# Optimization experiments

Measured on AMD Instinct MI355X. Metric: run time of the kernel, lower is better.

The kernel has to match this reference:

```python
import jax, jax.numpy as jnp
import numpy as np

B, H, SQ, SK, D = 2, 16, 2048, 2048, 128
SCALE = 0.20884964425119185
P_DROP = 0.125

def setup_inputs() -> dict:
    key = jax.random.key(0)
    k1, k2, k3 = jax.random.split(key, 3)
    x1 = jax.random.normal(k1, (B, H, SQ, D), dtype=jnp.float32)
    x2 = jax.random.normal(k2, (B, H, SK, D), dtype=jnp.float32)
    # inverted dropout mask: 0 with prob p, else 1/(1-p)
    keep = jax.random.uniform(k3, (B, H, SQ, SK)) >= P_DROP
    dropout_mask = keep.astype(jnp.float32) / (1.0 - P_DROP)
    return {"x1": x1, "x2": x2, "dropout_mask": dropout_mask}

def reference(x1, x2, dropout_mask):
    # scores: [B,H,Sq,Sk]
    scores = jnp.einsum('bhqd,bhkd->bhqk', x1, x2) * SCALE
    attn = jax.nn.softmax(scores, axis=-1)
    attn = attn * dropout_mask
    # output: [B,H,Sq,D]
    return jnp.einsum('bhqk,bhkd->bhqd', attn, x2)
```

## Files before the change

kernel.cpp:

```cpp
#include <hip/hip_runtime.h>
#include <hip/hip_bf16.h>

#define SQ 2048
#define SK 2048
#define DD 128
#define NBH 32
#define QBLK 64
#define KBLK 32
#define NKT (SK / KBLK)
#define SCALE 0.20884964425119185f
#define SCL2 (SCALE * 1.4426950408889634f)

typedef __attribute__((ext_vector_type(8))) short short8;
typedef __attribute__((ext_vector_type(4))) float f32x4;
typedef __attribute__((ext_vector_type(4))) unsigned int u32x4;

#define KIMG 8192
#define SMEM_BF 32768
#define KPITCH 272
#define VPITCH 80
#define VOFF_F 8704
#define SMEM_F32 18944

#define GLDS(G, L) __builtin_amdgcn_global_load_lds( \
    (const __attribute__((address_space(1))) unsigned int*)(G), \
    (__attribute__((address_space(3))) unsigned int*)(L), 16, 0, 0)

static __device__ __forceinline__ unsigned int pk_bf16(float lo, float hi) {
    float2 f2; f2.x = lo; f2.y = hi;
    __hip_bfloat162 h = __float22bfloat162_rn(f2);
    union { __hip_bfloat162 h2; unsigned int u; } cv; cv.h2 = h;
    return cv.u;
}

#define SOFTMAX_NAT(PA, SA_, SB_, MCa, MCb, LPART)                             \
  { float p_[8];                                                               \
    p_[0] = __builtin_amdgcn_exp2f(SA_[0]*SCL2);                               \
    p_[1] = __builtin_amdgcn_exp2f(SA_[1]*SCL2);                               \
    p_[2] = __builtin_amdgcn_exp2f(SA_[2]*SCL2);                               \
    p_[3] = __builtin_amdgcn_exp2f(SA_[3]*SCL2);                               \
    p_[4] = __builtin_amdgcn_exp2f(SB_[0]*SCL2);                               \
    p_[5] = __builtin_amdgcn_exp2f(SB_[1]*SCL2);                               \
    p_[6] = __builtin_amdgcn_exp2f(SB_[2]*SCL2);                               \
    p_[7] = __builtin_amdgcn_exp2f(SB_[3]*SCL2);                               \
    LPART += ((p_[0]+p_[1]) + (p_[2]+p_[3])) + ((p_[4]+p_[5]) + (p_[6]+p_[7]));\
    p_[0]*=MCa.x; p_[1]*=MCa.y; p_[2]*=MCa.z; p_[3]*=MCa.w;                    \
    p_[4]*=MCb.x; p_[5]*=MCb.y; p_[6]*=MCb.z; p_[7]*=MCb.w;                    \
    union { unsigned int u[4]; short8 v; } pb_;                                \
    pb_.u[0] = pk_bf16(p_[0],p_[1]); pb_.u[1] = pk_bf16(p_[2],p_[3]);          \
    pb_.u[2] = pk_bf16(p_[4],p_[5]); pb_.u[3] = pk_bf16(p_[6],p_[7]);          \
    PA = pb_.v; }

#define SOFTMAX_PACK(PA, SA_, SB_, MCa, MCb, LPART)                            \
  { float p_[8];                                                               \
    p_[0] = __builtin_amdgcn_exp2f(SA_[0]*SCL2);                               \
    p_[1] = __builtin_amdgcn_exp2f(SA_[1]*SCL2);                               \
    p_[2] = __builtin_amdgcn_exp2f(SA_[2]*SCL2);                               \
    p_[3] = __builtin_amdgcn_exp2f(SA_[3]*SCL2);                               \
    p_[4] = __builtin_amdgcn_exp2f(SB_[0]*SCL2);                               \
    p_[5] = __builtin_amdgcn_exp2f(SB_[1]*SCL2);                               \
    p_[6] = __builtin_amdgcn_exp2f(SB_[2]*SCL2);                               \
    p_[7] = __builtin_amdgcn_exp2f(SB_[3]*SCL2);                               \
    LPART += ((p_[0]+p_[1]) + (p_[2]+p_[3])) + ((p_[4]+p_[5]) + (p_[6]+p_[7]));\
    p_[0]*=MCa.x; p_[1]*=MCa.y; p_[2]*=MCa.z; p_[3]*=MCa.w;                    \
    p_[4]*=MCb.x; p_[5]*=MCb.y; p_[6]*=MCb.z; p_[7]*=MCb.w;                    \
    unsigned int P0 = pk_bf16(p_[0],p_[1]), P1 = pk_bf16(p_[2],p_[3]);         \
    unsigned int P2 = pk_bf16(p_[4],p_[5]), P3 = pk_bf16(p_[6],p_[7]);         \
    unsigned int a0 = __shfl((int)P0, sA), a2 = __shfl((int)P2, sA);           \
    unsigned int b0 = __shfl((int)P1, sA), b2 = __shfl((int)P3, sA);           \
    unsigned int c0 = __shfl((int)P0, sB), c2 = __shfl((int)P2, sB);           \
    unsigned int d0 = __shfl((int)P1, sB), d2 = __shfl((int)P3, sB);           \
    union { unsigned int u[4]; short8 v; } pb_;                                \
    pb_.u[0] = hi ? a2 : a0; pb_.u[1] = hi ? b2 : b0;                          \
    pb_.u[2] = hi ? c2 : c0; pb_.u[3] = hi ? d2 : d0;                          \
    PA = pb_.v; }

#define BAR()                                                                  \
    asm volatile("s_waitcnt lgkmcnt(0)" ::: "memory");                         \
    __builtin_amdgcn_sched_barrier(0);                                         \
    __builtin_amdgcn_s_barrier();                                              \
    __builtin_amdgcn_sched_barrier(0);

#define VBAR()                                                                 \
    asm volatile("s_waitcnt vmcnt(0)" ::: "memory");                           \
    __builtin_amdgcn_sched_barrier(0);                                         \
    __builtin_amdgcn_s_barrier();                                              \
    __builtin_amdgcn_sched_barrier(0);

#define BODY_BF(CUR, OTH, MC0, MC1, MN0, MN1, KT)                              \
  { const int ktn = ((KT) < NKT - 1) ? (KT) + 1 : (KT);                        \
    const unsigned char* gK = wsKb + (size_t)ktn * KIMG + tid * 16;            \
    const unsigned char* gV = wsVb + (size_t)ktn * KIMG + tid * 16;            \
    GLDS(gK,        smem + (OTH)*KIMG + (wid << 10));                          \
    GLDS(gK + 4096, smem + (OTH)*KIMG + 4096 + (wid << 10));                   \
    GLDS(gV,        smem + 16384 + (OTH)*KIMG + (wid << 10));                  \
    GLDS(gV + 4096, smem + 16384 + (OTH)*KIMG + 4096 + (wid << 10));           \
    MN0 = *(const float4*)(mq0 + ktn * KBLK);                                  \
    MN1 = *(const float4*)(mq0 + ktn * KBLK + 16);                             \
    f32x4 s00 = {0,0,0,0}, s01 = {0,0,0,0};                                    \
    __builtin_amdgcn_s_setprio(1);                                             \
    _Pragma("unroll")                                                          \
    for (int ks = 0; ks < 4; ++ks) {                                           \
      short8 ka0 = *(const short8*)(smem + (CUR)*KIMG + kaddr[ks]);            \
      short8 ka1 = *(const short8*)(smem + (CUR)*KIMG + 4096 + kaddr[ks]);     \
      s00 = __builtin_amdgcn_mfma_f32_16x16x32_bf16(ka0, qf[ks], s00, 0,0,0);  \
      s01 = __builtin_amdgcn_mfma_f32_16x16x32_bf16(ka1, qf[ks], s01, 0,0,0);  \
    }                                                                          \
    __builtin_amdgcn_s_setprio(0);                                             \
    short8 pa;                                                                 \
    SOFTMAX_NAT(pa, s00, s01, MC0, MC1, lp)                                    \
    __builtin_amdgcn_s_setprio(1);                                             \
    _Pragma("unroll")                                                          \
    for (int d8 = 0; d8 < 8; ++d8) {                                           \
      short8 vv = *(const short8*)(smem + 16384 + (CUR)*KIMG                   \
                                   + (d8*16 + c)*64 + 16*g);                   \
      o[d8] = __builtin_amdgcn_mfma_f32_16x16x32_bf16(pa, vv, o[d8], 0,0,0);   \
    }                                                                          \
    __builtin_amdgcn_s_setprio(0);                                             \
    VBAR() }

#define KERNEL_PRE(SMEMSZ)                                                     \
    __shared__ __align__(16) unsigned char smem[SMEMSZ];                       \
    const int tid  = threadIdx.x;                                              \
    const int lane = tid & 63, wid = tid >> 6;                                 \
    const int c = lane & 15, g = lane >> 4;                                    \
    const int bid = blockIdx.x;                                                \
    const int swz = (bid & 7) * 128 + (bid >> 3);  \
    const int bh = swz >> 5;                                                   \
    const int qb = swz & 31;                                                   \
    const float* x1b = x1 + ((size_t)bh * SQ + (size_t)qb * QBLK) * DD;        \
    const float* mb  = mask + ((size_t)bh * SQ + (size_t)qb * QBLK) * SK;      \
    float*      outb = out + ((size_t)bh * SQ + (size_t)qb * QBLK) * DD;       \
    const int sA = c + ((g & 1) << 5);                                         \
    const int sB = sA + 16;                                                    \
    const bool hi = (g >= 2);                                                  \
    const float* mq0 = mb + (size_t)(wid*16 + c) * SK + 4*g;

#define KERNEL_QLOAD()                                                         \
    short8 qf[4];                                                              \
    {  const float* q0r = x1b + (size_t)(wid*16 + c) * DD;                     \
       _Pragma("unroll")                                                       \
       for (int ks = 0; ks < 4; ++ks) {                                        \
           float4 a = *(const float4*)(q0r + ks*32 + 8*g);                     \
           float4 b = *(const float4*)(q0r + ks*32 + 8*g + 4);                 \
           union { unsigned int u[4]; short8 s; } t;                           \
           t.u[0]=pk_bf16(a.x,a.y); t.u[1]=pk_bf16(a.z,a.w);                   \
           t.u[2]=pk_bf16(b.x,b.y); t.u[3]=pk_bf16(b.z,b.w);                   \
           qf[ks]=t.s;                                                         \
       } }

#define KERNEL_EPILOGUE()                                                      \
    float l = lp; l += __shfl_xor(l, 16); l += __shfl_xor(l, 32);              \
    float il0 = 1.0f/__shfl(l, 4*g+0), il1 = 1.0f/__shfl(l, 4*g+1);            \
    float il2 = 1.0f/__shfl(l, 4*g+2), il3 = 1.0f/__shfl(l, 4*g+3);            \
    float* orow = outb + (size_t)(wid*16) * DD;                                \
    _Pragma("unroll")                                                          \
    for (int d8 = 0; d8 < 8; ++d8) {                                           \
        orow[(4*g + 0) * DD + d8*16 + c] = o[d8][0] * il0;                     \
        orow[(4*g + 1) * DD + d8*16 + c] = o[d8][1] * il1;                     \
        orow[(4*g + 2) * DD + d8*16 + c] = o[d8][2] * il2;                     \
        orow[(4*g + 3) * DD + d8*16 + c] = o[d8][3] * il3;                     \
    }

__global__ __launch_bounds__(256) void prep_kv(const float* __restrict__ x2,
                                               unsigned char* __restrict__ wsK,
                                               unsigned char* __restrict__ wsV) {
    __shared__ unsigned short lt[128 * 34];
    const int blk = blockIdx.x;
    const int bh = blk >> 6, kt = blk & 63;
    const int t = threadIdx.x;
    const int r = t >> 3, dc = t & 7;
    const float* src = x2 + ((size_t)bh * SK + (size_t)(kt * 32 + r)) * DD + dc * 16;
    float4 a0 = *(const float4*)(src);
    float4 a1 = *(const float4*)(src + 4);
    float4 a2 = *(const float4*)(src + 8);
    float4 a3 = *(const float4*)(src + 12);
    u32x4 w0, w1;
    w0[0]=pk_bf16(a0.x,a0.y); w0[1]=pk_bf16(a0.z,a0.w);
    w0[2]=pk_bf16(a1.x,a1.y); w0[3]=pk_bf16(a1.z,a1.w);
    w1[0]=pk_bf16(a2.x,a2.y); w1[1]=pk_bf16(a2.z,a2.w);
    w1[2]=pk_bf16(a3.x,a3.y); w1[3]=pk_bf16(a3.z,a3.w);
    const int A0 = 64*(dc>>1) + 16*((2*dc)   & 3);
    const int A1 = 64*(dc>>1) + 16*((2*dc+1) & 3);
    const int keyr = 16 * (r & 7);
    unsigned char* dstK = wsK + ((size_t)bh*64 + kt) * KIMG + r * 256;
    *(u32x4*)(dstK + (A0 ^ keyr)) = w0;
    *(u32x4*)(dstK + (A1 ^ keyr)) = w1;
    const int tt = r & 15;
    const int s = 8*(tt>>2) + 4*(r>>4) + (tt&3);
#pragma unroll
    for (int i = 0; i < 4; ++i) {
        unsigned int u = w0[i];
        lt[(dc*16 + 2*i    ) * 34 + s] = (unsigned short)(u & 0xffffu);
        lt[(dc*16 + 2*i + 1) * 34 + s] = (unsigned short)(u >> 16);
    }
#pragma unroll
    for (int i = 0; i < 4; ++i) {
        unsigned int u = w1[i];
        lt[(dc*16 + 8 + 2*i    ) * 34 + s] = (unsigned short)(u & 0xffffu);
        lt[(dc*16 + 8 + 2*i + 1) * 34 + s] = (unsigned short)(u >> 16);
    }
    __syncthreads();
    const int d = t >> 1, h = t & 1;
    const unsigned int* lrow = (const unsigned int*)((const unsigned char*)lt + d*68 + h*32);
    u32x4 o0, o1;
    o0[0]=lrow[0]; o0[1]=lrow[1]; o0[2]=lrow[2]; o0[3]=lrow[3];
    o1[0]=lrow[4]; o1[1]=lrow[5]; o1[2]=lrow[6]; o1[3]=lrow[7];
    unsigned char* dstV = wsV + ((size_t)bh*64 + kt) * KIMG + d*64 + h*32;
    *(u32x4*)(dstV)      = o0;
    *(u32x4*)(dstV + 16) = o1;
}

__global__ __launch_bounds__(256, 4) void fattn_bf16(
    const float* __restrict__ x1, const unsigned char* __restrict__ wsK,
    const unsigned char* __restrict__ wsV,
    const float* __restrict__ mask, float* __restrict__ out)
{
    KERNEL_PRE(SMEM_BF)
    const unsigned char* wsKb = wsK + (size_t)bh * 64 * KIMG;
    const unsigned char* wsVb = wsV + (size_t)bh * 64 * KIMG;
    const int key = 16 * (c & 7);
    int kaddr[4];
#pragma unroll
    for (int ks = 0; ks < 4; ++ks)
        kaddr[ks] = c * 256 + ((ks * 64 + 16 * g) ^ key);

    GLDS(wsKb + tid * 16,        smem + (wid << 10));
    GLDS(wsKb + 4096 + tid * 16, smem + 4096 + (wid << 10));
    GLDS(wsVb + tid * 16,        smem + 16384 + (wid << 10));
    GLDS(wsVb + 4096 + tid * 16, smem + 16384 + 4096 + (wid << 10));
    float4 mA0 = *(const float4*)(mq0);
    float4 mA1 = *(const float4*)(mq0 + 16);
    float4 mB0, mB1;
    KERNEL_QLOAD()
    VBAR()

    f32x4 o[8] = {};
    float lp = 0.f;

    for (int kt2 = 0; kt2 < NKT / 2; ++kt2) {
        BODY_BF(0, 1, mA0, mA1, mB0, mB1, 2*kt2)
        BODY_BF(1, 0, mB0, mB1, mA0, mA1, 2*kt2 + 1)
    }
    KERNEL_EPILOGUE()
}

#define BODY_F32(KC0,KC1,KC2,KC3, VC0,VC1,VC2,VC3, MC0,MC1,                    \
                 KN0,KN1,KN2,KN3, VN0,VN1,VN2,VN3, MN0,MN1, KT)                \
  { const int kbn = ((KT) < NKT - 1) ? ((KT) + 1) * KBLK : (KT) * KBLK;        \
    KN0 = *(const float4*)(x2fb + (size_t)(kbn + kkf)      * DD + kd0);        \
    KN1 = *(const float4*)(x2fb + (size_t)(kbn + kkf)      * DD + kd0 + 4);    \
    KN2 = *(const float4*)(x2fb + (size_t)(kbn + kkf + 16) * DD + kd0);        \
    KN3 = *(const float4*)(x2fb + (size_t)(kbn + kkf + 16) * DD + kd0 + 4);    \
    VN0 = *(const float4*)(x2fb + (size_t)(kbn + 2*kp)     * DD + vdb);        \
    VN1 = *(const float4*)(x2fb + (size_t)(kbn + 2*kp)     * DD + vdb + 4);    \
    VN2 = *(const float4*)(x2fb + (size_t)(kbn + 2*kp + 1) * DD + vdb);        \
    VN3 = *(const float4*)(x2fb + (size_t)(kbn + 2*kp + 1) * DD + vdb + 4);    \
    MN0 = *(const float4*)(mq0 + kbn);                                         \
    MN1 = *(const float4*)(mq0 + kbn + 16);                                    \
    { union { unsigned int u[4]; short8 s; } k0_, k1_;                         \
      k0_.u[0]=pk_bf16(KC0.x,KC0.y); k0_.u[1]=pk_bf16(KC0.z,KC0.w);            \
      k0_.u[2]=pk_bf16(KC1.x,KC1.y); k0_.u[3]=pk_bf16(KC1.z,KC1.w);            \
      k1_.u[0]=pk_bf16(KC2.x,KC2.y); k1_.u[1]=pk_bf16(KC2.z,KC2.w);            \
      k1_.u[2]=pk_bf16(KC3.x,KC3.y); k1_.u[3]=pk_bf16(KC3.z,KC3.w);            \
      *(short8*)(smem + (kkf)      * KPITCH + 2*kd0) = k0_.s;                  \
      *(short8*)(smem + (kkf + 16) * KPITCH + 2*kd0) = k1_.s; }                \
    *(unsigned int*)(smem + VOFF_F + (vdb+0)*VPITCH + 4*kp) = pk_bf16(VC0.x, VC2.x); \
    *(unsigned int*)(smem + VOFF_F + (vdb+1)*VPITCH + 4*kp) = pk_bf16(VC0.y, VC2.y); \
    *(unsigned int*)(smem + VOFF_F + (vdb+2)*VPITCH + 4*kp) = pk_bf16(VC0.z, VC2.z); \
    *(unsigned int*)(smem + VOFF_F + (vdb+3)*VPITCH + 4*kp) = pk_bf16(VC0.w, VC2.w); \
    *(unsigned int*)(smem + VOFF_F + (vdb+4)*VPITCH + 4*kp) = pk_bf16(VC1.x, VC3.x); \
    *(unsigned int*)(smem + VOFF_F + (vdb+5)*VPITCH + 4*kp) = pk_bf16(VC1.y, VC3.y); \
    *(unsigned int*)(smem + VOFF_F + (vdb+6)*VPITCH + 4*kp) = pk_bf16(VC1.z, VC3.z); \
    *(unsigned int*)(smem + VOFF_F + (vdb+7)*VPITCH + 4*kp) = pk_bf16(VC1.w, VC3.w); \
    BAR()                                                                      \
    f32x4 s00={0,0,0,0}, s01={0,0,0,0};                                        \
    _Pragma("unroll")                                                          \
    for (int ks = 0; ks < 4; ++ks) {                                           \
      short8 ka0 = *(const short8*)(smem + (c)      * KPITCH + ks*64 + 16*g);  \
      short8 ka1 = *(const short8*)(smem + (16 + c) * KPITCH + ks*64 + 16*g);  \
      s00 = __builtin_amdgcn_mfma_f32_16x16x32_bf16(ka0, qf[ks], s00, 0,0,0);  \
      s01 = __builtin_amdgcn_mfma_f32_16x16x32_bf16(ka1, qf[ks], s01, 0,0,0);  \
    }                                                                          \
    short8 pa;                                                                 \
    SOFTMAX_PACK(pa, s00, s01, MC0, MC1, lp)                                   \
    _Pragma("unroll")                                                          \
    for (int d8 = 0; d8 < 8; ++d8) {                                           \
      short8 vv = *(const short8*)(smem + VOFF_F + (d8*16 + c)*VPITCH + 16*g); \
      o[d8] = __builtin_amdgcn_mfma_f32_16x16x32_bf16(pa, vv, o[d8], 0,0,0);   \
    }                                                                          \
    BAR()                                                                      \
  }

__global__ __launch_bounds__(256, 3) void fattn_f32(
    const float* __restrict__ x1, const float* __restrict__ x2,
    const float* __restrict__ mask, float* __restrict__ out)
{
    KERNEL_PRE(SMEM_F32)
    const float* x2fb = x2 + (size_t)bh * SK * DD;
    const int kkf = tid >> 4, kd0 = (tid & 15) * 8;
    const int kp  = tid & 15, vdb = (tid >> 4) * 8;

    float4 kA0 = *(const float4*)(x2fb + (size_t)(kkf)      * DD + kd0);
    float4 kA1 = *(const float4*)(x2fb + (size_t)(kkf)      * DD + kd0 + 4);
    float4 kA2 = *(const float4*)(x2fb + (size_t)(kkf + 16) * DD + kd0);
    float4 kA3 = *(const float4*)(x2fb + (size_t)(kkf + 16) * DD + kd0 + 4);
    float4 vA0 = *(const float4*)(x2fb + (size_t)(2*kp)     * DD + vdb);
    float4 vA1 = *(const float4*)(x2fb + (size_t)(2*kp)     * DD + vdb + 4);
    float4 vA2 = *(const float4*)(x2fb + (size_t)(2*kp + 1) * DD + vdb);
    float4 vA3 = *(const float4*)(x2fb + (size_t)(2*kp + 1) * DD + vdb + 4);
    float4 mA0 = *(const float4*)(mq0);
    float4 mA1 = *(const float4*)(mq0 + 16);
    float4 kB0,kB1,kB2,kB3, vB0,vB1,vB2,vB3, mB0,mB1;

    KERNEL_QLOAD()

    f32x4 o[8] = {};
    float lp = 0.f;

    for (int kt2 = 0; kt2 < NKT / 2; ++kt2) {
        BODY_F32(kA0,kA1,kA2,kA3, vA0,vA1,vA2,vA3, mA0,mA1,
                 kB0,kB1,kB2,kB3, vB0,vB1,vB2,vB3, mB0,mB1, 2*kt2)
        BODY_F32(kB0,kB1,kB2,kB3, vB0,vB1,vB2,vB3, mB0,mB1,
                 kA0,kA1,kA2,kA3, vA0,vA1,vA2,vA3, mA0,mA1, 2*kt2 + 1)
    }
    KERNEL_EPILOGUE()
}

extern "C" void kernel_launch(void* const* d_in, const int* in_sizes, int n_in,
                              void* d_out, int out_size, void* d_ws, size_t ws_size,
                              hipStream_t stream) {
    const float* x1   = (const float*)d_in[0];
    const float* x2   = (const float*)d_in[1];
    const float* mask = (const float*)d_in[2];
    float* out = (float*)d_out;
    const size_t szK = (size_t)NBH * 64 * KIMG;
    const size_t szV = (size_t)NBH * 64 * KIMG;
    if (ws_size >= szK + szV) {
        unsigned char* wsK = (unsigned char*)d_ws;
        unsigned char* wsV = wsK + szK;
        prep_kv<<<dim3(NBH * 64), dim3(256), 0, stream>>>(x2, wsK, wsV);
        fattn_bf16<<<dim3(NBH * (SQ / QBLK)), dim3(256), 0, stream>>>(
            x1, wsK, wsV, mask, out);
    } else {
        fattn_f32<<<dim3(NBH * (SQ / QBLK)), dim3(256), 0, stream>>>(x1, x2, mask, out);
    }
}
```

Before: 190.5 us.

## Load K/V fragments directly from global into registers, dropping LDS staging

The bf16 attention kernel no longer stages K and V tiles into shared memory via global_load_lds with barriers. The pre-pass now writes K in an MFMA-fragment layout so each lane reads its short8 operands straight from global (L2) into registers, with K for the next tile prefetched after the QK MFMAs. This removes LDS traffic and the per-tile block barrier, but adds more register pressure (occupancy lowered to 3 waves), and the global loads of V sit in front of the PV MFMAs. Each wave now also loads the K/V data that used to be shared across the block through LDS, which increases L2 traffic.

```diff
diff --git a/kernel.cpp b/kernel.cpp
--- a/kernel.cpp
+++ b/kernel.cpp
@@ -16,15 +16,10 @@
 typedef __attribute__((ext_vector_type(4))) unsigned int u32x4;
 
 #define KIMG 8192
-#define SMEM_BF 32768
 #define KPITCH 272
 #define VPITCH 80
 #define VOFF_F 8704
 #define SMEM_F32 18944
-
-#define GLDS(G, L) __builtin_amdgcn_global_load_lds( \
-    (const __attribute__((address_space(1))) unsigned int*)(G), \
-    (__attribute__((address_space(3))) unsigned int*)(L), 16, 0, 0)
 
 static __device__ __forceinline__ unsigned int pk_bf16(float lo, float hi) {
     float2 f2; f2.x = lo; f2.y = hi;
@@ -81,46 +76,35 @@
     __builtin_amdgcn_s_barrier();                                              \
     __builtin_amdgcn_sched_barrier(0);
 
-#define VBAR()                                                                 \
-    asm volatile("s_waitcnt vmcnt(0)" ::: "memory");                           \
-    __builtin_amdgcn_sched_barrier(0);                                         \
-    __builtin_amdgcn_s_barrier();                                              \
-    __builtin_amdgcn_sched_barrier(0);
-
-#define BODY_BF(CUR, OTH, MC0, MC1, MN0, MN1, KT)                              \
-  { const int ktn = ((KT) < NKT - 1) ? (KT) + 1 : (KT);                        \
-    const unsigned char* gK = wsKb + (size_t)ktn * KIMG + tid * 16;            \
-    const unsigned char* gV = wsVb + (size_t)ktn * KIMG + tid * 16;            \
-    GLDS(gK,        smem + (OTH)*KIMG + (wid << 10));                          \
-    GLDS(gK + 4096, smem + (OTH)*KIMG + 4096 + (wid << 10));                   \
-    GLDS(gV,        smem + 16384 + (OTH)*KIMG + (wid << 10));                  \
-    GLDS(gV + 4096, smem + 16384 + (OTH)*KIMG + 4096 + (wid << 10));           \
-    MN0 = *(const float4*)(mq0 + ktn * KBLK);                                  \
-    MN1 = *(const float4*)(mq0 + ktn * KBLK + 16);                             \
+#define BODY_BF(MC0, MC1, MN0, MN1, KT)                                        \
+  { const size_t tb  = (size_t)(KT) * KIMG;                                    \
+    const size_t tbn = (size_t)(((KT) < NKT - 1) ? (KT) + 1 : (KT)) * KIMG;    \
+    _Pragma("unroll")                                                          \
+    for (int d8 = 0; d8 < 8; ++d8)                                             \
+      vf[d8] = *(const short8*)(vbase + tb + d8 * 1024);                       \
     f32x4 s00 = {0,0,0,0}, s01 = {0,0,0,0};                                    \
     __builtin_amdgcn_s_setprio(1);                                             \
     _Pragma("unroll")                                                          \
     for (int ks = 0; ks < 4; ++ks) {                                           \
-      short8 ka0 = *(const short8*)(smem + (CUR)*KIMG + kaddr[ks]);            \
-      short8 ka1 = *(const short8*)(smem + (CUR)*KIMG + 4096 + kaddr[ks]);     \
-      s00 = __builtin_amdgcn_mfma_f32_16x16x32_bf16(ka0, qf[ks], s00, 0,0,0);  \
-      s01 = __builtin_amdgcn_mfma_f32_16x16x32_bf16(ka1, qf[ks], s01, 0,0,0);  \
+      s00 = __builtin_amdgcn_mfma_f32_16x16x32_bf16(kf[2*ks],   qf[ks], s00, 0,0,0); \
+      s01 = __builtin_amdgcn_mfma_f32_16x16x32_bf16(kf[2*ks+1], qf[ks], s01, 0,0,0); \
     }                                                                          \
     __builtin_amdgcn_s_setprio(0);                                             \
+    _Pragma("unroll")                                                          \
+    for (int f = 0; f < 8; ++f)                                                \
+      kf[f] = *(const short8*)(kbase + tbn + f * 1024);                        \
+    MN0 = *(const float4*)(mq0 + (((KT) < NKT - 1) ? (KT) + 1 : (KT)) * KBLK); \
+    MN1 = *(const float4*)(mq0 + (((KT) < NKT - 1) ? (KT) + 1 : (KT)) * KBLK + 16); \
     short8 pa;                                                                 \
     SOFTMAX_NAT(pa, s00, s01, MC0, MC1, lp)                                    \
     __builtin_amdgcn_s_setprio(1);                                             \
     _Pragma("unroll")                                                          \
-    for (int d8 = 0; d8 < 8; ++d8) {                                           \
-      short8 vv = *(const short8*)(smem + 16384 + (CUR)*KIMG                   \
-                                   + (d8*16 + c)*64 + 16*g);                   \
-      o[d8] = __builtin_amdgcn_mfma_f32_16x16x32_bf16(pa, vv, o[d8], 0,0,0);   \
-    }                                                                          \
+    for (int d8 = 0; d8 < 8; ++d8)                                             \
+      o[d8] = __builtin_amdgcn_mfma_f32_16x16x32_bf16(pa, vf[d8], o[d8], 0,0,0); \
     __builtin_amdgcn_s_setprio(0);                                             \
-    VBAR() }
-
-#define KERNEL_PRE(SMEMSZ)                                                     \
-    __shared__ __align__(16) unsigned char smem[SMEMSZ];                       \
+  }
+
+#define KERNEL_PRE()                                                           \
     const int tid  = threadIdx.x;                                              \
     const int lane = tid & 63, wid = tid >> 6;                                 \
     const int c = lane & 15, g = lane >> 4;                                    \
@@ -131,9 +115,6 @@
     const float* x1b = x1 + ((size_t)bh * SQ + (size_t)qb * QBLK) * DD;        \
     const float* mb  = mask + ((size_t)bh * SQ + (size_t)qb * QBLK) * SK;      \
     float*      outb = out + ((size_t)bh * SQ + (size_t)qb * QBLK) * DD;       \
-    const int sA = c + ((g & 1) << 5);                                         \
-    const int sB = sA + 16;                                                    \
-    const bool hi = (g >= 2);                                                  \
     const float* mq0 = mb + (size_t)(wid*16 + c) * SK + 4*g;
 
 #define KERNEL_QLOAD()                                                         \
@@ -180,12 +161,13 @@
     w0[2]=pk_bf16(a1.x,a1.y); w0[3]=pk_bf16(a1.z,a1.w);
     w1[0]=pk_bf16(a2.x,a2.y); w1[1]=pk_bf16(a2.z,a2.w);
     w1[2]=pk_bf16(a3.x,a3.y); w1[3]=pk_bf16(a3.z,a3.w);
-    const int A0 = 64*(dc>>1) + 16*((2*dc)   & 3);
-    const int A1 = 64*(dc>>1) + 16*((2*dc+1) & 3);
-    const int keyr = 16 * (r & 7);
-    unsigned char* dstK = wsK + ((size_t)bh*64 + kt) * KIMG + r * 256;
-    *(u32x4*)(dstK + (A0 ^ keyr)) = w0;
-    *(u32x4*)(dstK + (A1 ^ keyr)) = w1;
+    {
+        const int f  = (dc >> 1) * 2 + (r >> 4);
+        const int a  = f * 1024 + (r & 15) * 64 + ((2 * dc) & 3) * 16;
+        unsigned char* dstK = wsK + ((size_t)bh * 64 + kt) * KIMG + a;
+        *(u32x4*)(dstK)      = w0;
+        *(u32x4*)(dstK + 16) = w1;
+    }
     const int tt = r & 15;
     const int s = 8*(tt>>2) + 4*(r>>4) + (tt&3);
 #pragma unroll
@@ -211,36 +193,31 @@
     *(u32x4*)(dstV + 16) = o1;
 }
 
-__global__ __launch_bounds__(256, 4) void fattn_bf16(
+__global__ __launch_bounds__(256, 3) void fattn_bf16(
     const float* __restrict__ x1, const unsigned char* __restrict__ wsK,
     const unsigned char* __restrict__ wsV,
     const float* __restrict__ mask, float* __restrict__ out)
 {
-    KERNEL_PRE(SMEM_BF)
-    const unsigned char* wsKb = wsK + (size_t)bh * 64 * KIMG;
-    const unsigned char* wsVb = wsV + (size_t)bh * 64 * KIMG;
-    const int key = 16 * (c & 7);
-    int kaddr[4];
+    KERNEL_PRE()
+    const unsigned char* kbase = wsK + (size_t)bh * 64 * KIMG + c * 64 + g * 16;
+    const unsigned char* vbase = wsV + (size_t)bh * 64 * KIMG + c * 64 + g * 16;
+
+    short8 kf[8], vf[8];
 #pragma unroll
-    for (int ks = 0; ks < 4; ++ks)
-        kaddr[ks] = c * 256 + ((ks * 64 + 16 * g) ^ key);
-
-    GLDS(wsKb + tid * 16,        smem + (wid << 10));
-    GLDS(wsKb + 4096 + tid * 16, smem + 4096 + (wid << 10));
-    GLDS(wsVb + tid * 16,        smem + 16384 + (wid << 10));
-    GLDS(wsVb + 4096 + tid * 16, smem + 16384 + 4096 + (wid << 10));
+    for (int f = 0; f < 8; ++f)
+        kf[f] = *(const short8*)(kbase + f * 1024);
     float4 mA0 = *(const float4*)(mq0);
     float4 mA1 = *(const float4*)(mq0 + 16);
     float4 mB0, mB1;
+
     KERNEL_QLOAD()
-    VBAR()
 
     f32x4 o[8] = {};
     float lp = 0.f;
 
     for (int kt2 = 0; kt2 < NKT / 2; ++kt2) {
-        BODY_BF(0, 1, mA0, mA1, mB0, mB1, 2*kt2)
-        BODY_BF(1, 0, mB0, mB1, mA0, mA1, 2*kt2 + 1)
+        BODY_BF(mA0, mA1, mB0, mB1, 2*kt2)
+        BODY_BF(mB0, mB1, mA0, mA1, 2*kt2 + 1)
     }
     KERNEL_EPILOGUE()
 }
@@ -296,7 +273,11 @@
     const float* __restrict__ x1, const float* __restrict__ x2,
     const float* __restrict__ mask, float* __restrict__ out)
 {
-    KERNEL_PRE(SMEM_F32)
+    __shared__ __align__(16) unsigned char smem[SMEM_F32];
+    KERNEL_PRE()
+    const int sA = c + ((g & 1) << 5);
+    const int sB = sA + 16;
+    const bool hi = (g >= 2);
     const float* x2fb = x2 + (size_t)bh * SK * DD;
     const int kkf = tid >> 4, kd0 = (tid & 15) * 8;
     const int kp  = tid & 15, vdb = (tid >> 4) * 8;
```

Result: slower. 325.2 us (+70.7%).

## Pre-swizzle K/V workspace into per-lane fragment order and relax end-of-tile wait

Applied to the files above, without the earlier changes.

The prep kernel now writes K and V bf16 tiles in the exact order the MFMA fragments are consumed, so each lane reads a contiguous 16-byte slot at lane*16 plus a fixed offset. This drops the XOR swizzle address math and should avoid LDS bank conflicts. The per-tile barrier now waits with vmcnt(2) instead of vmcnt(0), so the next tile's mask loads can stay in flight across the barrier while the global-to-LDS copies must complete. This depends on the vmcnt ordering of those loads being correct.

```diff
diff --git a/kernel.cpp b/kernel.cpp
--- a/kernel.cpp
+++ b/kernel.cpp
@@ -81,12 +81,6 @@
     __builtin_amdgcn_s_barrier();                                              \
     __builtin_amdgcn_sched_barrier(0);
 
-#define VBAR()                                                                 \
-    asm volatile("s_waitcnt vmcnt(0)" ::: "memory");                           \
-    __builtin_amdgcn_sched_barrier(0);                                         \
-    __builtin_amdgcn_s_barrier();                                              \
-    __builtin_amdgcn_sched_barrier(0);
-
 #define BODY_BF(CUR, OTH, MC0, MC1, MN0, MN1, KT)                              \
   { const int ktn = ((KT) < NKT - 1) ? (KT) + 1 : (KT);                        \
     const unsigned char* gK = wsKb + (size_t)ktn * KIMG + tid * 16;            \
@@ -95,14 +89,15 @@
     GLDS(gK + 4096, smem + (OTH)*KIMG + 4096 + (wid << 10));                   \
     GLDS(gV,        smem + 16384 + (OTH)*KIMG + (wid << 10));                  \
     GLDS(gV + 4096, smem + 16384 + (OTH)*KIMG + 4096 + (wid << 10));           \
+    __builtin_amdgcn_sched_barrier(0);           \
     MN0 = *(const float4*)(mq0 + ktn * KBLK);                                  \
     MN1 = *(const float4*)(mq0 + ktn * KBLK + 16);                             \
     f32x4 s00 = {0,0,0,0}, s01 = {0,0,0,0};                                    \
     __builtin_amdgcn_s_setprio(1);                                             \
     _Pragma("unroll")                                                          \
     for (int ks = 0; ks < 4; ++ks) {                                           \
-      short8 ka0 = *(const short8*)(smem + (CUR)*KIMG + kaddr[ks]);            \
-      short8 ka1 = *(const short8*)(smem + (CUR)*KIMG + 4096 + kaddr[ks]);     \
+      short8 ka0 = *(const short8*)(smem + (CUR)*KIMG + (2*ks)*1024 + lb);     \
+      short8 ka1 = *(const short8*)(smem + (CUR)*KIMG + (2*ks+1)*1024 + lb);   \
       s00 = __builtin_amdgcn_mfma_f32_16x16x32_bf16(ka0, qf[ks], s00, 0,0,0);  \
       s01 = __builtin_amdgcn_mfma_f32_16x16x32_bf16(ka1, qf[ks], s01, 0,0,0);  \
     }                                                                          \
@@ -112,20 +107,25 @@
     __builtin_amdgcn_s_setprio(1);                                             \
     _Pragma("unroll")                                                          \
     for (int d8 = 0; d8 < 8; ++d8) {                                           \
-      short8 vv = *(const short8*)(smem + 16384 + (CUR)*KIMG                   \
-                                   + (d8*16 + c)*64 + 16*g);                   \
+      short8 vv = *(const short8*)(smem + 16384 + (CUR)*KIMG + d8*1024 + lb);  \
       o[d8] = __builtin_amdgcn_mfma_f32_16x16x32_bf16(pa, vv, o[d8], 0,0,0);   \
     }                                                                          \
     __builtin_amdgcn_s_setprio(0);                                             \
-    VBAR() }
+    __builtin_amdgcn_sched_barrier(0);                                         \
+    asm volatile("s_waitcnt vmcnt(2)" ::: "memory");                           \
+    __builtin_amdgcn_sched_barrier(0);                                         \
+    __builtin_amdgcn_s_barrier();                                              \
+    __builtin_amdgcn_sched_barrier(0);                                         \
+  }
 
 #define KERNEL_PRE(SMEMSZ)                                                     \
     __shared__ __align__(16) unsigned char smem[SMEMSZ];                       \
     const int tid  = threadIdx.x;                                              \
     const int lane = tid & 63, wid = tid >> 6;                                 \
     const int c = lane & 15, g = lane >> 4;                                    \
+    const int lb = lane * 16;                                                  \
     const int bid = blockIdx.x;                                                \
-    const int swz = (bid & 7) * 128 + (bid >> 3);  \
+    const int swz = (bid & 7) * 128 + (bid >> 3);          \
     const int bh = swz >> 5;                                                   \
     const int qb = swz & 31;                                                   \
     const float* x1b = x1 + ((size_t)bh * SQ + (size_t)qb * QBLK) * DD;        \
@@ -134,7 +134,8 @@
     const int sA = c + ((g & 1) << 5);                                         \
     const int sB = sA + 16;                                                    \
     const bool hi = (g >= 2);                                                  \
-    const float* mq0 = mb + (size_t)(wid*16 + c) * SK + 4*g;
+    const float* mq0 = mb + (size_t)(wid*16 + c) * SK + 4*g;                   \
+    (void)sA; (void)sB; (void)hi; (void)lb;
 
 #define KERNEL_QLOAD()                                                         \
     short8 qf[4];                                                              \
@@ -180,12 +181,13 @@
     w0[2]=pk_bf16(a1.x,a1.y); w0[3]=pk_bf16(a1.z,a1.w);
     w1[0]=pk_bf16(a2.x,a2.y); w1[1]=pk_bf16(a2.z,a2.w);
     w1[2]=pk_bf16(a3.x,a3.y); w1[3]=pk_bf16(a3.z,a3.w);
-    const int A0 = 64*(dc>>1) + 16*((2*dc)   & 3);
-    const int A1 = 64*(dc>>1) + 16*((2*dc+1) & 3);
-    const int keyr = 16 * (r & 7);
-    unsigned char* dstK = wsK + ((size_t)bh*64 + kt) * KIMG + r * 256;
-    *(u32x4*)(dstK + (A0 ^ keyr)) = w0;
-    *(u32x4*)(dstK + (A1 ^ keyr)) = w1;
+    {
+        const int ks = dc >> 1, rh = r >> 4, f = 2*ks + rh;
+        const int cl = r & 15, g0 = 2 * (dc & 1);
+        unsigned char* dstK = wsK + ((size_t)bh * 64 + kt) * KIMG + f * 1024 + cl * 16;
+        *(u32x4*)(dstK + (g0)     * 256) = w0;
+        *(u32x4*)(dstK + (g0 + 1) * 256) = w1;
+    }
     const int tt = r & 15;
     const int s = 8*(tt>>2) + 4*(r>>4) + (tt&3);
 #pragma unroll
@@ -202,13 +204,15 @@
     }
     __syncthreads();
     const int d = t >> 1, h = t & 1;
+    const int d8 = d >> 4, cl = d & 15;
     const unsigned int* lrow = (const unsigned int*)((const unsigned char*)lt + d*68 + h*32);
     u32x4 o0, o1;
     o0[0]=lrow[0]; o0[1]=lrow[1]; o0[2]=lrow[2]; o0[3]=lrow[3];
     o1[0]=lrow[4]; o1[1]=lrow[5]; o1[2]=lrow[6]; o1[3]=lrow[7];
-    unsigned char* dstV = wsV + ((size_t)bh*64 + kt) * KIMG + d*64 + h*32;
-    *(u32x4*)(dstV)      = o0;
-    *(u32x4*)(dstV + 16) = o1;
+    unsigned char* dstV = wsV + ((size_t)bh*64 + kt) * KIMG + d8*1024
+                        + (2*h)*256 + cl*16;
+    *(u32x4*)(dstV)       = o0;
+    *(u32x4*)(dstV + 256) = o1;
 }
 
 __global__ __launch_bounds__(256, 4) void fattn_bf16(
@@ -219,11 +223,6 @@
     KERNEL_PRE(SMEM_BF)
     const unsigned char* wsKb = wsK + (size_t)bh * 64 * KIMG;
     const unsigned char* wsVb = wsV + (size_t)bh * 64 * KIMG;
-    const int key = 16 * (c & 7);
-    int kaddr[4];
-#pragma unroll
-    for (int ks = 0; ks < 4; ++ks)
-        kaddr[ks] = c * 256 + ((ks * 64 + 16 * g) ^ key);
 
     GLDS(wsKb + tid * 16,        smem + (wid << 10));
     GLDS(wsKb + 4096 + tid * 16, smem + 4096 + (wid << 10));
@@ -233,7 +232,10 @@
     float4 mA1 = *(const float4*)(mq0 + 16);
     float4 mB0, mB1;
     KERNEL_QLOAD()
-    VBAR()
+    asm volatile("s_waitcnt vmcnt(0)" ::: "memory");
+    __builtin_amdgcn_sched_barrier(0);
+    __builtin_amdgcn_s_barrier();
+    __builtin_amdgcn_sched_barrier(0);
 
     f32x4 o[8] = {};
     float lp = 0.f;
```

Result: no change. 188.8 us (-0.9%).
